# Performance work log

Measured on AMD Instinct MI355X. Metric: run time of the kernel, lower is better.

Reference implementation:

```python
import jax, jax.numpy as jnp
import numpy as np

HIDDEN = 1024
HEADS = 16
HEAD_DIM = HIDDEN // HEADS


def setup_inputs() -> dict:
    key = jax.random.key(0)
    ks = jax.random.split(key, 4)
    B, S, H = 2, 2048, HIDDEN
    scale = 1.0 / np.sqrt(H)
    return {
        "inputs": jax.random.normal(ks[0], (B, S, H), dtype=jnp.float32),
        "mask": jnp.ones((B, S), dtype=jnp.int32),
        "Wq": jax.random.normal(ks[1], (H, H), dtype=jnp.float32) * scale,
        "bq": jnp.zeros((H,), dtype=jnp.float32),
        "Wk": jax.random.normal(ks[2], (H, H), dtype=jnp.float32) * scale,
        "bk": jnp.zeros((H,), dtype=jnp.float32),
        "Wv": jax.random.normal(ks[3], (H, H), dtype=jnp.float32) * scale,
        "bv": jnp.zeros((H,), dtype=jnp.float32),
    }


def _split_heads(x, B, S):
    # [B,S,H] -> [B,heads,S,head_dim]
    return x.reshape(B, S, HEADS, HEAD_DIM).transpose(0, 2, 1, 3)


def reference(inputs, mask, Wq, bq, Wk, bk, Wv, bv):
    B, S, H = inputs.shape
    q = _split_heads(inputs @ Wq.T + bq, B, S)
    k = _split_heads(inputs @ Wk.T + bk, B, S)
    v = _split_heads(inputs @ Wv.T + bv, B, S)
    scores = jnp.einsum("bhqd,bhkd->bhqk", q, k) / jnp.sqrt(
        jnp.asarray(HEAD_DIM, dtype=inputs.dtype))
    # mask broadcast [B,1,1,S]; zeros -> -inf
    scores = jnp.where(mask[:, None, None, :] == 0, -jnp.inf, scores)
    attn = jax.nn.softmax(scores, axis=-1)
    context = jnp.einsum("bhqk,bhkd->bhqd", attn, v)
    return context.transpose(0, 2, 1, 3).reshape(B, S, H)
```

## Files before the change

kernel.cpp:

```cpp
#include <hip/hip_runtime.h>
#include <hip/hip_fp16.h>

constexpr int S_LEN  = 2048;
constexpr int HID    = 1024;
constexpr int HEADS  = 16;
constexpr int HDIM   = 64;
constexpr int BATCH  = 2;
constexpr int BH     = BATCH * HEADS;
constexpr int M_ROWS = BATCH * S_LEN;

typedef _Float16 half8  __attribute__((ext_vector_type(8)));
typedef _Float16 half4v __attribute__((ext_vector_type(4)));
typedef _Float16 half2v __attribute__((ext_vector_type(2)));
typedef float    f32x4  __attribute__((ext_vector_type(4)));

constexpr float EXP2_OFF = -11.541560327111707f;
constexpr float Q_SCALE  = 0.18033688011112042f;

__global__ __launch_bounds__(256) void cvt_kernel(
    const float* __restrict__ X,  const float* __restrict__ Wq,
    const float* __restrict__ Wk, const float* __restrict__ Wv,
    const int* __restrict__ mask,
    _Float16* __restrict__ Xh,  _Float16* __restrict__ Wqh,
    _Float16* __restrict__ Wkh, _Float16* __restrict__ Wvh,
    float* __restrict__ maskF)
{
    const int blk = blockIdx.x;
    if (blk >= 3584) {
        const int loc = blk - 3584;
        const size_t e = ((size_t)loc * 256 + threadIdx.x) * 8;
        #pragma unroll
        for (int i = 0; i < 8; ++i)
            maskF[e + i] = mask[e + i] ? EXP2_OFF : -1.0e30f;
        return;
    }
    const float* src; _Float16* dst; int loc;
    if (blk < 2048)      { src = X;  dst = Xh;  loc = blk; }
    else if (blk < 2560) { src = Wq; dst = Wqh; loc = blk - 2048; }
    else if (blk < 3072) { src = Wk; dst = Wkh; loc = blk - 2560; }
    else                 { src = Wv; dst = Wvh; loc = blk - 3072; }
    const size_t e = ((size_t)loc * 256 + threadIdx.x) * 8;
    float4 a = *reinterpret_cast<const float4*>(&src[e]);
    float4 b = *reinterpret_cast<const float4*>(&src[e + 4]);
    half8 h = { (_Float16)a.x, (_Float16)a.y, (_Float16)a.z, (_Float16)a.w,
                (_Float16)b.x, (_Float16)b.y, (_Float16)b.z, (_Float16)b.w };
    *reinterpret_cast<half8*>(&dst[e]) = h;
}

__device__ __forceinline__ void async_cp16(_Float16* lds, const _Float16* g) {
    __builtin_amdgcn_global_load_lds(
        (const __attribute__((address_space(1))) void*)g,
        (__attribute__((address_space(3))) void*)lds, 16, 0, 0);
}

__global__ __launch_bounds__(256) void qkv_proj_kernel(
    const _Float16* __restrict__ Xh,
    const _Float16* __restrict__ Wqh, const _Float16* __restrict__ Wkh,
    const _Float16* __restrict__ Wvh,
    const float* __restrict__ bq, const float* __restrict__ bk,
    const float* __restrict__ bv,
    _Float16* __restrict__ Qo, _Float16* __restrict__ Ko,
    _Float16* __restrict__ Vo)
{
    const int mode = blockIdx.z;
    const _Float16* W    = (mode == 0) ? Wqh : (mode == 1) ? Wkh : Wvh;
    const float*    bias = (mode == 0) ? bq  : (mode == 1) ? bk  : bv;
    _Float16*       Out  = (mode == 0) ? Qo  : (mode == 1) ? Ko  : Vo;

    const int m0 = blockIdx.x * 128, n0 = blockIdx.y * 128;
    const int tid = threadIdx.x, wave = tid >> 6, lane = tid & 63;
    const int l15 = lane & 15, quad = lane >> 4;

    __shared__ _Float16 As[128 * 64];
    __shared__ _Float16 Bs[128 * 64];

    f32x4 acc[4][4];
    #pragma unroll
    for (int mt = 0; mt < 4; ++mt)
        #pragma unroll
        for (int nt = 0; nt < 4; ++nt) acc[mt][nt] = (f32x4){0.f, 0.f, 0.f, 0.f};

    const int wm = (wave & 1) * 64, wn = (wave >> 1) * 64;

    for (int k0 = 0; k0 < HID; k0 += 64) {
        #pragma unroll
        for (int i = 0; i < 4; ++i) {
            const int chunk = wave * 4 + i;
            const int row   = chunk * 8 + (lane >> 3);
            const int lofs  = chunk * 512 + lane * 8;
            const int scol  = (lane & 7) * 8;
            async_cp16(&As[lofs], &Xh[(size_t)(m0 + row) * HID + k0 + scol]);
            async_cp16(&Bs[lofs], &W [(size_t)(n0 + row) * HID + k0 + scol]);
        }
        __syncthreads();

        #pragma unroll
        for (int c = 0; c < 2; ++c) {
            half8 af[4], bf[4];
            #pragma unroll
            for (int mt = 0; mt < 4; ++mt)
                af[mt] = *reinterpret_cast<const half8*>(
                    &As[(wm + mt * 16 + l15) * 64 + c * 32 + quad * 8]);
            #pragma unroll
            for (int nt = 0; nt < 4; ++nt)
                bf[nt] = *reinterpret_cast<const half8*>(
                    &Bs[(wn + nt * 16 + l15) * 64 + c * 32 + quad * 8]);
            #pragma unroll
            for (int mt = 0; mt < 4; ++mt)
                #pragma unroll
                for (int nt = 0; nt < 4; ++nt)
                    acc[mt][nt] = __builtin_amdgcn_mfma_f32_16x16x32_f16(
                        af[mt], bf[nt], acc[mt][nt], 0, 0, 0);
        }
        __syncthreads();
    }

    #pragma unroll
    for (int nt = 0; nt < 4; ++nt) {
        const int n = n0 + wn + nt * 16 + l15;
        const float bias_n = bias[n];
        const int h = n >> 6, d = n & 63;
        #pragma unroll
        for (int mt = 0; mt < 4; ++mt) {
            #pragma unroll
            for (int r = 0; r < 4; ++r) {
                const int m = m0 + wm + mt * 16 + quad * 4 + r;
                const int b = m >> 11, s = m & 2047;
                const int bh = b * HEADS + h;
                float v = acc[mt][nt][r] + bias_n;
                if (mode == 0) v *= Q_SCALE;
                Out[((size_t)bh * S_LEN + s) * HDIM + d] = (_Float16)v;
            }
        }
    }
}

__global__ __launch_bounds__(256) void vtrans_kernel(
    const _Float16* __restrict__ V, _Float16* __restrict__ Vt)
{
    __shared__ _Float16 T[64][72];
    const int bh = blockIdx.y, s0 = blockIdx.x * 64, tid = threadIdx.x;

    const _Float16* src = V + ((size_t)bh * S_LEN + s0) * HDIM;
    #pragma unroll
    for (int i = 0; i < 2; ++i) {
        const int slot = tid + i * 256;
        const int row = slot >> 3, c8 = (slot & 7) * 8;
        half8 v = *reinterpret_cast<const half8*>(&src[row * HDIM + c8]);
        #pragma unroll
        for (int j = 0; j < 8; ++j) T[c8 + j][row] = v[j];
    }
    __syncthreads();

    _Float16* dst = Vt + (size_t)bh * HDIM * S_LEN + s0;
    #pragma unroll
    for (int i = 0; i < 2; ++i) {
        const int slot = tid + i * 256;
        const int d = slot >> 3, s8 = (slot & 7) * 8;
        half8 v = *reinterpret_cast<const half8*>(&T[d][s8]);
        *reinterpret_cast<half8*>(&dst[(size_t)d * S_LEN + s8]) = v;
    }
}

__global__ __launch_bounds__(256) void attn_kernel(
    const _Float16* __restrict__ Q, const _Float16* __restrict__ K,
    const _Float16* __restrict__ Vt, const float* __restrict__ maskF,
    float* __restrict__ Out)
{
    const int id    = blockIdx.x;
    const int xcd   = id & 7, local = id >> 3;
    const int bh    = xcd * 4 + (local & 3);
    const int qt    = local >> 2;
    const int b = bh >> 4, h = bh & 15;
    const int tid = threadIdx.x, wave = tid >> 6, lane = tid & 63;
    const int l15 = lane & 15, quad = lane >> 4;

    __shared__ _Float16 Ks[2][64 * 64];
    __shared__ _Float16 Vs[2][64 * 64];
    __shared__ _Float16 Ps[4][2][16][68];

    const _Float16* Qb = Q  + (size_t)bh * S_LEN * HDIM;
    const _Float16* Kb = K  + (size_t)bh * S_LEN * HDIM;
    const _Float16* Vb = Vt + (size_t)bh * HDIM * S_LEN;
    const float*    mb = maskF + b * S_LEN;

    half8 qf[2][2];
    #pragma unroll
    for (int rs = 0; rs < 2; ++rs) {
        const int qrow = qt * 128 + wave * 32 + rs * 16 + l15;
        qf[rs][0] = *reinterpret_cast<const half8*>(&Qb[(size_t)qrow * HDIM + quad * 8]);
        qf[rs][1] = *reinterpret_cast<const half8*>(&Qb[(size_t)qrow * HDIM + 32 + quad * 8]);
    }

    f32x4 acc[2][4];
    #pragma unroll
    for (int rs = 0; rs < 2; ++rs)
        #pragma unroll
        for (int mt = 0; mt < 4; ++mt) acc[rs][mt] = (f32x4){0.f, 0.f, 0.f, 0.f};
    float den[2] = {0.f, 0.f};

    const int srow = lane >> 3;
    const int scol = (lane & 7) * 8;
    auto stage = [&](int kb, int buf) {
        #pragma unroll
        for (int j = 0; j < 2; ++j) {
            const int r0   = wave * 16 + j * 8;
            const int lofs = r0 * 64 + lane * 8;
            async_cp16(&Ks[buf][lofs],
                       &Kb[(size_t)(kb + r0 + srow) * HDIM + scol]);
            async_cp16(&Vs[buf][lofs],
                       &Vb[(size_t)(r0 + srow) * S_LEN + kb + scol]);
        }
    };

    stage(0, 0);
    int buf = 0;

    for (int kb = 0; kb < S_LEN; kb += 64) {
        __syncthreads();
        if (kb + 64 < S_LEN) stage(kb + 64, buf ^ 1);

        float4 m4[4];
        #pragma unroll
        for (int nt = 0; nt < 4; ++nt)
            m4[nt] = *reinterpret_cast<const float4*>(&mb[kb + nt * 16 + quad * 4]);

        half8 kf[2][4];
        #pragma unroll
        for (int c = 0; c < 2; ++c)
            #pragma unroll
            for (int nt = 0; nt < 4; ++nt)
                kf[c][nt] = *reinterpret_cast<const half8*>(
                    &Ks[buf][(nt * 16 + l15) * 64 + c * 32 + quad * 8]);
        f32x4 sc[2][4];
        #pragma unroll
        for (int rs = 0; rs < 2; ++rs)
            #pragma unroll
            for (int nt = 0; nt < 4; ++nt) sc[rs][nt] = (f32x4){0.f, 0.f, 0.f, 0.f};
        #pragma unroll
        for (int c = 0; c < 2; ++c)
            #pragma unroll
            for (int nt = 0; nt < 4; ++nt)
                #pragma unroll
                for (int rs = 0; rs < 2; ++rs)
                    sc[rs][nt] = __builtin_amdgcn_mfma_f32_16x16x32_f16(
                        kf[c][nt], qf[rs][c], sc[rs][nt], 0, 0, 0);

        half8 vf[2][4];
        #pragma unroll
        for (int c = 0; c < 2; ++c)
            #pragma unroll
            for (int mt = 0; mt < 4; ++mt)
                vf[c][mt] = *reinterpret_cast<const half8*>(
                    &Vs[buf][(mt * 16 + l15) * 64 + c * 32 + quad * 8]);

        #pragma unroll
        for (int rs = 0; rs < 2; ++rs)
            #pragma unroll
            for (int nt = 0; nt < 4; ++nt) {
                float p0 = __builtin_amdgcn_exp2f(sc[rs][nt][0] + m4[nt].x);
                float p1 = __builtin_amdgcn_exp2f(sc[rs][nt][1] + m4[nt].y);
                float p2 = __builtin_amdgcn_exp2f(sc[rs][nt][2] + m4[nt].z);
                float p3 = __builtin_amdgcn_exp2f(sc[rs][nt][3] + m4[nt].w);
                den[rs] += (p0 + p1) + (p2 + p3);
                half2v lo = __builtin_bit_cast(half2v, __builtin_amdgcn_cvt_pkrtz(p0, p1));
                half2v hi = __builtin_bit_cast(half2v, __builtin_amdgcn_cvt_pkrtz(p2, p3));
                half4v pk = { lo[0], lo[1], hi[0], hi[1] };
                *reinterpret_cast<half4v*>(&Ps[wave][rs][l15][nt * 16 + quad * 4]) = pk;
            }
        asm volatile("s_waitcnt lgkmcnt(0)" ::: "memory");

        #pragma unroll
        for (int rs = 0; rs < 2; ++rs) {
            #pragma unroll
            for (int c = 0; c < 2; ++c) {
                half4v plo = *reinterpret_cast<const half4v*>(
                    &Ps[wave][rs][l15][c * 32 + quad * 8]);
                half4v phi = *reinterpret_cast<const half4v*>(
                    &Ps[wave][rs][l15][c * 32 + quad * 8 + 4]);
                half8 pf = { plo[0], plo[1], plo[2], plo[3],
                             phi[0], phi[1], phi[2], phi[3] };
                #pragma unroll
                for (int mt = 0; mt < 4; ++mt)
                    acc[rs][mt] = __builtin_amdgcn_mfma_f32_16x16x32_f16(
                        vf[c][mt], pf, acc[rs][mt], 0, 0, 0);
            }
        }
        buf ^= 1;
    }

    #pragma unroll
    for (int rs = 0; rs < 2; ++rs) {
        den[rs] += __shfl_xor(den[rs], 16, 64);
        den[rs] += __shfl_xor(den[rs], 32, 64);
        den[rs] = 1.0f / den[rs];
    }

    #pragma unroll
    for (int rs = 0; rs < 2; ++rs) {
        const int qrow = qt * 128 + wave * 32 + rs * 16 + l15;
        float* orow = Out + ((size_t)(b * S_LEN + qrow)) * HID + h * HDIM;
        #pragma unroll
        for (int mt = 0; mt < 4; ++mt) {
            float4 o = { acc[rs][mt][0] * den[rs], acc[rs][mt][1] * den[rs],
                         acc[rs][mt][2] * den[rs], acc[rs][mt][3] * den[rs] };
            *reinterpret_cast<float4*>(&orow[mt * 16 + quad * 4]) = o;
        }
    }
}

extern "C" void kernel_launch(void* const* d_in, const int* in_sizes, int n_in,
                              void* d_out, int out_size, void* d_ws, size_t ws_size,
                              hipStream_t stream) {
    const float* X  = (const float*)d_in[0];
    const int*   mk = (const int*)  d_in[1];
    const float* Wq = (const float*)d_in[2];
    const float* bq = (const float*)d_in[3];
    const float* Wk = (const float*)d_in[4];
    const float* bk = (const float*)d_in[5];
    const float* Wv = (const float*)d_in[6];
    const float* bv = (const float*)d_in[7];
    float* out = (float*)d_out;

    _Float16* XhVt = (_Float16*)d_ws;
    _Float16* Wqh  = XhVt + (size_t)M_ROWS * HID;
    _Float16* Wkh  = Wqh + (size_t)HID * HID;
    _Float16* Wvh  = Wkh + (size_t)HID * HID;
    _Float16* Q    = Wvh + (size_t)HID * HID;
    _Float16* K    = Q   + (size_t)BH * S_LEN * HDIM;
    _Float16* Vo   = K   + (size_t)BH * S_LEN * HDIM;
    float*    maskF = (float*)(Vo + (size_t)BH * S_LEN * HDIM);

    cvt_kernel<<<3586, 256, 0, stream>>>(X, Wq, Wk, Wv, mk, XhVt, Wqh, Wkh, Wvh, maskF);

    dim3 gp(M_ROWS / 128, HID / 128, 3);
    qkv_proj_kernel<<<gp, 256, 0, stream>>>(XhVt, Wqh, Wkh, Wvh, bq, bk, bv, Q, K, Vo);

    dim3 gt(S_LEN / 64, BH);
    vtrans_kernel<<<gt, 256, 0, stream>>>(Vo, XhVt);

    attn_kernel<<<512, 256, 0, stream>>>(Q, K, XhVt, maskF, out);
}
```

Before: 201.7 us.

## Use eight waves of 16 query rows and XOR-swizzle K/V shared tiles

The attention kernel now runs 512 threads per block, with each of eight waves owning 16 query rows instead of four waves owning 32 rows. Each thread stages one 16-byte chunk of K and of V per tile. The shared-memory K/V layout is XOR-swizzled by row to avoid LDS bank conflicts on fragment reads. This cuts per-wave register use and increases the number of waves available to hide latency, but each K/V fragment load is now amortized over half as many MFMAs, which raises LDS read traffic.

```diff
diff --git a/kernel.cpp b/kernel.cpp
--- a/kernel.cpp
+++ b/kernel.cpp
@@ -162,7 +162,7 @@
     }
 }
 
-__global__ __launch_bounds__(256) void attn_kernel(
+__global__ __launch_bounds__(512) void attn_kernel(
     const _Float16* __restrict__ Q, const _Float16* __restrict__ K,
     const _Float16* __restrict__ Vt, const float* __restrict__ maskF,
     float* __restrict__ Out)
@@ -177,44 +177,35 @@
 
     __shared__ _Float16 Ks[2][64 * 64];
     __shared__ _Float16 Vs[2][64 * 64];
-    __shared__ _Float16 Ps[4][2][16][68];
+    __shared__ _Float16 Ps[8][16][68];
 
     const _Float16* Qb = Q  + (size_t)bh * S_LEN * HDIM;
     const _Float16* Kb = K  + (size_t)bh * S_LEN * HDIM;
     const _Float16* Vb = Vt + (size_t)bh * HDIM * S_LEN;
     const float*    mb = maskF + b * S_LEN;
 
-    half8 qf[2][2];
-    #pragma unroll
-    for (int rs = 0; rs < 2; ++rs) {
-        const int qrow = qt * 128 + wave * 32 + rs * 16 + l15;
-        qf[rs][0] = *reinterpret_cast<const half8*>(&Qb[(size_t)qrow * HDIM + quad * 8]);
-        qf[rs][1] = *reinterpret_cast<const half8*>(&Qb[(size_t)qrow * HDIM + 32 + quad * 8]);
-    }
-
-    f32x4 acc[2][4];
-    #pragma unroll
-    for (int rs = 0; rs < 2; ++rs)
-        #pragma unroll
-        for (int mt = 0; mt < 4; ++mt) acc[rs][mt] = (f32x4){0.f, 0.f, 0.f, 0.f};
-    float den[2] = {0.f, 0.f};
-
-    const int srow = lane >> 3;
-    const int scol = (lane & 7) * 8;
+    const int qrow = qt * 128 + wave * 16 + l15;
+    half8 qf[2];
+    qf[0] = *reinterpret_cast<const half8*>(&Qb[(size_t)qrow * HDIM + quad * 8]);
+    qf[1] = *reinterpret_cast<const half8*>(&Qb[(size_t)qrow * HDIM + 32 + quad * 8]);
+
+    f32x4 acc[4];
+    #pragma unroll
+    for (int mt = 0; mt < 4; ++mt) acc[mt] = (f32x4){0.f, 0.f, 0.f, 0.f};
+    float den = 0.f;
+
+    const int srow_t  = tid >> 3;
+    const int schunk  = (tid & 7) ^ (srow_t & 7);
     auto stage = [&](int kb, int buf) {
-        #pragma unroll
-        for (int j = 0; j < 2; ++j) {
-            const int r0   = wave * 16 + j * 8;
-            const int lofs = r0 * 64 + lane * 8;
-            async_cp16(&Ks[buf][lofs],
-                       &Kb[(size_t)(kb + r0 + srow) * HDIM + scol]);
-            async_cp16(&Vs[buf][lofs],
-                       &Vb[(size_t)(r0 + srow) * S_LEN + kb + scol]);
-        }
+        async_cp16(&Ks[buf][tid * 8],
+                   &Kb[(size_t)(kb + srow_t) * HDIM + schunk * 8]);
+        async_cp16(&Vs[buf][tid * 8],
+                   &Vb[(size_t)srow_t * S_LEN + kb + schunk * 8]);
     };
 
     stage(0, 0);
     int buf = 0;
+    const int rsw = (l15 & 7);
 
     for (int kb = 0; kb < S_LEN; kb += 64) {
         __syncthreads();
@@ -231,20 +222,16 @@
             #pragma unroll
             for (int nt = 0; nt < 4; ++nt)
                 kf[c][nt] = *reinterpret_cast<const half8*>(
-                    &Ks[buf][(nt * 16 + l15) * 64 + c * 32 + quad * 8]);
-        f32x4 sc[2][4];
-        #pragma unroll
-        for (int rs = 0; rs < 2; ++rs)
-            #pragma unroll
-            for (int nt = 0; nt < 4; ++nt) sc[rs][nt] = (f32x4){0.f, 0.f, 0.f, 0.f};
+                    &Ks[buf][(nt * 16 + l15) * 64 + ((c * 4 + quad) ^ rsw) * 8]);
+        f32x4 sc[4];
+        #pragma unroll
+        for (int nt = 0; nt < 4; ++nt) sc[nt] = (f32x4){0.f, 0.f, 0.f, 0.f};
         #pragma unroll
         for (int c = 0; c < 2; ++c)
             #pragma unroll
             for (int nt = 0; nt < 4; ++nt)
-                #pragma unroll
-                for (int rs = 0; rs < 2; ++rs)
-                    sc[rs][nt] = __builtin_amdgcn_mfma_f32_16x16x32_f16(
-                        kf[c][nt], qf[rs][c], sc[rs][nt], 0, 0, 0);
+                sc[nt] = __builtin_amdgcn_mfma_f32_16x16x32_f16(
+                    kf[c][nt], qf[c], sc[nt], 0, 0, 0);
 
         half8 vf[2][4];
         #pragma unroll
@@ -252,60 +239,48 @@
             #pragma unroll
             for (int mt = 0; mt < 4; ++mt)
                 vf[c][mt] = *reinterpret_cast<const half8*>(
-                    &Vs[buf][(mt * 16 + l15) * 64 + c * 32 + quad * 8]);
-
-        #pragma unroll
-        for (int rs = 0; rs < 2; ++rs)
-            #pragma unroll
-            for (int nt = 0; nt < 4; ++nt) {
-                float p0 = __builtin_amdgcn_exp2f(sc[rs][nt][0] + m4[nt].x);
-                float p1 = __builtin_amdgcn_exp2f(sc[rs][nt][1] + m4[nt].y);
-                float p2 = __builtin_amdgcn_exp2f(sc[rs][nt][2] + m4[nt].z);
-                float p3 = __builtin_amdgcn_exp2f(sc[rs][nt][3] + m4[nt].w);
-                den[rs] += (p0 + p1) + (p2 + p3);
-                half2v lo = __builtin_bit_cast(half2v, __builtin_amdgcn_cvt_pkrtz(p0, p1));
-                half2v hi = __builtin_bit_cast(half2v, __builtin_amdgcn_cvt_pkrtz(p2, p3));
-                half4v pk = { lo[0], lo[1], hi[0], hi[1] };
-                *reinterpret_cast<half4v*>(&Ps[wave][rs][l15][nt * 16 + quad * 4]) = pk;
-            }
+                    &Vs[buf][(mt * 16 + l15) * 64 + ((c * 4 + quad) ^ rsw) * 8]);
+
+        #pragma unroll
+        for (int nt = 0; nt < 4; ++nt) {
+            float p0 = __builtin_amdgcn_exp2f(sc[nt][0] + m4[nt].x);
+            float p1 = __builtin_amdgcn_exp2f(sc[nt][1] + m4[nt].y);
+            float p2 = __builtin_amdgcn_exp2f(sc[nt][2] + m4[nt].z);
+            float p3 = __builtin_amdgcn_exp2f(sc[nt][3] + m4[nt].w);
+            den += (p0 + p1) + (p2 + p3);
+            half2v lo = __builtin_bit_cast(half2v, __builtin_amdgcn_cvt_pkrtz(p0, p1));
+            half2v hi = __builtin_bit_cast(half2v, __builtin_amdgcn_cvt_pkrtz(p2, p3));
+            half4v pk = { lo[0], lo[1], hi[0], hi[1] };
+            *reinterpret_cast<half4v*>(&Ps[wave][l15][nt * 16 + quad * 4]) = pk;
+        }
         asm volatile("s_waitcnt lgkmcnt(0)" ::: "memory");
 
         #pragma unroll
-        for (int rs = 0; rs < 2; ++rs) {
-            #pragma unroll
-            for (int c = 0; c < 2; ++c) {
-                half4v plo = *reinterpret_cast<const half4v*>(
-                    &Ps[wave][rs][l15][c * 32 + quad * 8]);
-                half4v phi = *reinterpret_cast<const half4v*>(
-                    &Ps[wave][rs][l15][c * 32 + quad * 8 + 4]);
-                half8 pf = { plo[0], plo[1], plo[2], plo[3],
-                             phi[0], phi[1], phi[2], phi[3] };
-                #pragma unroll
-                for (int mt = 0; mt < 4; ++mt)
-                    acc[rs][mt] = __builtin_amdgcn_mfma_f32_16x16x32_f16(
-                        vf[c][mt], pf, acc[rs][mt], 0, 0, 0);
-            }
+        for (int c = 0; c < 2; ++c) {
+            half4v plo = *reinterpret_cast<const half4v*>(
+                &Ps[wave][l15][c * 32 + quad * 8]);
+            half4v phi = *reinterpret_cast<const half4v*>(
+                &Ps[wave][l15][c * 32 + quad * 8 + 4]);
+            half8 pf = { plo[0], plo[1], plo[2], plo[3],
+                         phi[0], phi[1], phi[2], phi[3] };
+            #pragma unroll
+            for (int mt = 0; mt < 4; ++mt)
+                acc[mt] = __builtin_amdgcn_mfma_f32_16x16x32_f16(
+                    vf[c][mt], pf, acc[mt], 0, 0, 0);
         }
         buf ^= 1;
     }
 
-    #pragma unroll
-    for (int rs = 0; rs < 2; ++rs) {
-        den[rs] += __shfl_xor(den[rs], 16, 64);
-        den[rs] += __shfl_xor(den[rs], 32, 64);
-        den[rs] = 1.0f / den[rs];
-    }
-
-    #pragma unroll
-    for (int rs = 0; rs < 2; ++rs) {
-        const int qrow = qt * 128 + wave * 32 + rs * 16 + l15;
-        float* orow = Out + ((size_t)(b * S_LEN + qrow)) * HID + h * HDIM;
-        #pragma unroll
-        for (int mt = 0; mt < 4; ++mt) {
-            float4 o = { acc[rs][mt][0] * den[rs], acc[rs][mt][1] * den[rs],
-                         acc[rs][mt][2] * den[rs], acc[rs][mt][3] * den[rs] };
-            *reinterpret_cast<float4*>(&orow[mt * 16 + quad * 4]) = o;
-        }
+    den += __shfl_xor(den, 16, 64);
+    den += __shfl_xor(den, 32, 64);
+    const float inv = 1.0f / den;
+
+    float* orow = Out + ((size_t)(b * S_LEN + qrow)) * HID + h * HDIM;
+    #pragma unroll
+    for (int mt = 0; mt < 4; ++mt) {
+        float4 o = { acc[mt][0] * inv, acc[mt][1] * inv,
+                     acc[mt][2] * inv, acc[mt][3] * inv };
+        *reinterpret_cast<float4*>(&orow[mt * 16 + quad * 4]) = o;
     }
 }
 
@@ -339,5 +314,5 @@
     dim3 gt(S_LEN / 64, BH);
     vtrans_kernel<<<gt, 256, 0, stream>>>(Vo, XhVt);
 
-    attn_kernel<<<512, 256, 0, stream>>>(Q, K, XhVt, maskF, out);
-}
+    attn_kernel<<<512, 512, 0, stream>>>(Q, K, XhVt, maskF, out);
+}
```

Measured after the change: 189.8 us. 1.06x faster.

## Fuse V transpose into QKV projection epilogue and swizzle attention LDS tiles

Applied to the files above, without the earlier changes.

The V projection blocks now transpose their output tile through shared memory and write V directly in [bh, d, s] layout, which removes the separate vtrans kernel launch and its extra global round trip. The attention kernel's K/V staging uses an XOR swizzle on 16-byte chunks, and the fragment reads apply the matching swizzle, to reduce LDS bank conflicts. The projection kernel's shared memory grows to hold the per-wave transpose buffers, which may lower occupancy. The transpose reuses LDS after the final __syncthreads and relies on an lgkmcnt wait rather than a barrier, which is only safe because each wave uses its own region.

```diff
diff --git a/kernel.cpp b/kernel.cpp
--- a/kernel.cpp
+++ b/kernel.cpp
@@ -60,19 +60,19 @@
     const float* __restrict__ bq, const float* __restrict__ bk,
     const float* __restrict__ bv,
     _Float16* __restrict__ Qo, _Float16* __restrict__ Ko,
-    _Float16* __restrict__ Vo)
+    _Float16* __restrict__ Vt)
 {
     const int mode = blockIdx.z;
     const _Float16* W    = (mode == 0) ? Wqh : (mode == 1) ? Wkh : Wvh;
     const float*    bias = (mode == 0) ? bq  : (mode == 1) ? bk  : bv;
-    _Float16*       Out  = (mode == 0) ? Qo  : (mode == 1) ? Ko  : Vo;
 
     const int m0 = blockIdx.x * 128, n0 = blockIdx.y * 128;
     const int tid = threadIdx.x, wave = tid >> 6, lane = tid & 63;
     const int l15 = lane & 15, quad = lane >> 4;
 
-    __shared__ _Float16 As[128 * 64];
-    __shared__ _Float16 Bs[128 * 64];
+    __shared__ _Float16 SMEM[18432];
+    _Float16* As = SMEM;
+    _Float16* Bs = SMEM + 8192;
 
     f32x4 acc[4][4];
     #pragma unroll
@@ -115,50 +115,54 @@
         __syncthreads();
     }
 
-    #pragma unroll
-    for (int nt = 0; nt < 4; ++nt) {
-        const int n = n0 + wn + nt * 16 + l15;
-        const float bias_n = bias[n];
-        const int h = n >> 6, d = n & 63;
-        #pragma unroll
-        for (int mt = 0; mt < 4; ++mt) {
-            #pragma unroll
-            for (int r = 0; r < 4; ++r) {
-                const int m = m0 + wm + mt * 16 + quad * 4 + r;
-                const int b = m >> 11, s = m & 2047;
-                const int bh = b * HEADS + h;
-                float v = acc[mt][nt][r] + bias_n;
-                if (mode == 0) v *= Q_SCALE;
-                Out[((size_t)bh * S_LEN + s) * HDIM + d] = (_Float16)v;
+    if (mode < 2) {
+        _Float16* Out = (mode == 0) ? Qo : Ko;
+        #pragma unroll
+        for (int nt = 0; nt < 4; ++nt) {
+            const int n = n0 + wn + nt * 16 + l15;
+            const float bias_n = bias[n];
+            const int h = n >> 6, d = n & 63;
+            #pragma unroll
+            for (int mt = 0; mt < 4; ++mt) {
+                #pragma unroll
+                for (int r = 0; r < 4; ++r) {
+                    const int m = m0 + wm + mt * 16 + quad * 4 + r;
+                    const int b = m >> 11, s = m & 2047;
+                    const int bh = b * HEADS + h;
+                    float v = acc[mt][nt][r] + bias_n;
+                    if (mode == 0) v *= Q_SCALE;
+                    Out[((size_t)bh * S_LEN + s) * HDIM + d] = (_Float16)v;
+                }
             }
         }
-    }
-}
-
-__global__ __launch_bounds__(256) void vtrans_kernel(
-    const _Float16* __restrict__ V, _Float16* __restrict__ Vt)
-{
-    __shared__ _Float16 T[64][72];
-    const int bh = blockIdx.y, s0 = blockIdx.x * 64, tid = threadIdx.x;
-
-    const _Float16* src = V + ((size_t)bh * S_LEN + s0) * HDIM;
-    #pragma unroll
-    for (int i = 0; i < 2; ++i) {
-        const int slot = tid + i * 256;
-        const int row = slot >> 3, c8 = (slot & 7) * 8;
-        half8 v = *reinterpret_cast<const half8*>(&src[row * HDIM + c8]);
-        #pragma unroll
-        for (int j = 0; j < 8; ++j) T[c8 + j][row] = v[j];
-    }
-    __syncthreads();
-
-    _Float16* dst = Vt + (size_t)bh * HDIM * S_LEN + s0;
-    #pragma unroll
-    for (int i = 0; i < 2; ++i) {
-        const int slot = tid + i * 256;
-        const int d = slot >> 3, s8 = (slot & 7) * 8;
-        half8 v = *reinterpret_cast<const half8*>(&T[d][s8]);
-        *reinterpret_cast<half8*>(&dst[(size_t)d * S_LEN + s8]) = v;
+    } else {
+        _Float16* T = SMEM + wave * 4608;
+        #pragma unroll
+        for (int nt = 0; nt < 4; ++nt) {
+            const int col = nt * 16 + l15;
+            const float bias_n = bias[n0 + wn + col];
+            #pragma unroll
+            for (int mt = 0; mt < 4; ++mt) {
+                half4v t = { (_Float16)(acc[mt][nt][0] + bias_n),
+                             (_Float16)(acc[mt][nt][1] + bias_n),
+                             (_Float16)(acc[mt][nt][2] + bias_n),
+                             (_Float16)(acc[mt][nt][3] + bias_n) };
+                *reinterpret_cast<half4v*>(&T[col * 72 + mt * 16 + quad * 4]) = t;
+            }
+        }
+        asm volatile("s_waitcnt lgkmcnt(0)" ::: "memory");
+        const int nn  = n0 + wn;
+        const int hh  = nn >> 6;
+        const int mm  = m0 + wm;
+        const int bb  = mm >> 11;
+        const int bhv = bb * HEADS + hh;
+        const int s0  = mm & 2047;
+        _Float16* dst = Vt + ((size_t)bhv * HDIM + lane) * S_LEN + s0;
+        #pragma unroll
+        for (int j = 0; j < 8; ++j) {
+            half8 v = *reinterpret_cast<const half8*>(&T[lane * 72 + j * 8]);
+            *reinterpret_cast<half8*>(&dst[j * 8]) = v;
+        }
     }
 }
 
@@ -199,22 +203,23 @@
         for (int mt = 0; mt < 4; ++mt) acc[rs][mt] = (f32x4){0.f, 0.f, 0.f, 0.f};
     float den[2] = {0.f, 0.f};
 
-    const int srow = lane >> 3;
-    const int scol = (lane & 7) * 8;
+    const int srow0    = tid >> 3;
+    const int chunkpos = tid & 7;
     auto stage = [&](int kb, int buf) {
         #pragma unroll
-        for (int j = 0; j < 2; ++j) {
-            const int r0   = wave * 16 + j * 8;
-            const int lofs = r0 * 64 + lane * 8;
-            async_cp16(&Ks[buf][lofs],
-                       &Kb[(size_t)(kb + r0 + srow) * HDIM + scol]);
-            async_cp16(&Vs[buf][lofs],
-                       &Vb[(size_t)(r0 + srow) * S_LEN + kb + scol]);
+        for (int hl = 0; hl < 2; ++hl) {
+            const int row = srow0 + hl * 32;
+            const int sch = chunkpos ^ (row & 7);
+            async_cp16(&Ks[buf][row * 64 + chunkpos * 8],
+                       &Kb[(size_t)(kb + row) * HDIM + sch * 8]);
+            async_cp16(&Vs[buf][row * 64 + chunkpos * 8],
+                       &Vb[(size_t)row * S_LEN + kb + sch * 8]);
         }
     };
 
     stage(0, 0);
     int buf = 0;
+    const int rsw = (l15 & 7);
 
     for (int kb = 0; kb < S_LEN; kb += 64) {
         __syncthreads();
@@ -231,7 +236,7 @@
             #pragma unroll
             for (int nt = 0; nt < 4; ++nt)
                 kf[c][nt] = *reinterpret_cast<const half8*>(
-                    &Ks[buf][(nt * 16 + l15) * 64 + c * 32 + quad * 8]);
+                    &Ks[buf][(nt * 16 + l15) * 64 + ((c * 4 + quad) ^ rsw) * 8]);
         f32x4 sc[2][4];
         #pragma unroll
         for (int rs = 0; rs < 2; ++rs)
@@ -252,7 +257,7 @@
             #pragma unroll
             for (int mt = 0; mt < 4; ++mt)
                 vf[c][mt] = *reinterpret_cast<const half8*>(
-                    &Vs[buf][(mt * 16 + l15) * 64 + c * 32 + quad * 8]);
+                    &Vs[buf][(mt * 16 + l15) * 64 + ((c * 4 + quad) ^ rsw) * 8]);
 
         #pragma unroll
         for (int rs = 0; rs < 2; ++rs)
@@ -322,22 +327,19 @@
     const float* bv = (const float*)d_in[7];
     float* out = (float*)d_out;
 
-    _Float16* XhVt = (_Float16*)d_ws;
-    _Float16* Wqh  = XhVt + (size_t)M_ROWS * HID;
-    _Float16* Wkh  = Wqh + (size_t)HID * HID;
-    _Float16* Wvh  = Wkh + (size_t)HID * HID;
-    _Float16* Q    = Wvh + (size_t)HID * HID;
-    _Float16* K    = Q   + (size_t)BH * S_LEN * HDIM;
-    _Float16* Vo   = K   + (size_t)BH * S_LEN * HDIM;
-    float*    maskF = (float*)(Vo + (size_t)BH * S_LEN * HDIM);
-
-    cvt_kernel<<<3586, 256, 0, stream>>>(X, Wq, Wk, Wv, mk, XhVt, Wqh, Wkh, Wvh, maskF);
+    _Float16* Xh  = (_Float16*)d_ws;
+    _Float16* Wqh = Xh  + (size_t)M_ROWS * HID;
+    _Float16* Wkh = Wqh + (size_t)HID * HID;
+    _Float16* Wvh = Wkh + (size_t)HID * HID;
+    _Float16* Q   = Wvh + (size_t)HID * HID;
+    _Float16* K   = Q   + (size_t)BH * S_LEN * HDIM;
+    _Float16* Vt  = K   + (size_t)BH * S_LEN * HDIM;
+    float*    maskF = (float*)(Vt + (size_t)BH * S_LEN * HDIM);
+
+    cvt_kernel<<<3586, 256, 0, stream>>>(X, Wq, Wk, Wv, mk, Xh, Wqh, Wkh, Wvh, maskF);
 
     dim3 gp(M_ROWS / 128, HID / 128, 3);
-    qkv_proj_kernel<<<gp, 256, 0, stream>>>(XhVt, Wqh, Wkh, Wvh, bq, bk, bv, Q, K, Vo);
-
-    dim3 gt(S_LEN / 64, BH);
-    vtrans_kernel<<<gt, 256, 0, stream>>>(Vo, XhVt);
-
-    attn_kernel<<<512, 256, 0, stream>>>(Q, K, XhVt, maskF, out);
-}
+    qkv_proj_kernel<<<gp, 256, 0, stream>>>(Xh, Wqh, Wkh, Wvh, bq, bk, bv, Q, K, Vt);
+
+    attn_kernel<<<512, 256, 0, stream>>>(Q, K, Vt, maskF, out);
+}
```

Measured after the change: 188.1 us. 1.07x faster.
